# Kernel optimization log

Measured on AMD Instinct MI355X. Metric: run time of the kernel, lower is better.

Reference implementation:

```python
import jax, jax.numpy as jnp
import numpy as np

N_NODES = 100000
N_EDGES = 6400000
N_GRAPHS = 64


def setup_inputs() -> dict:
    key = jax.random.key(0)
    k = jax.random.split(key, 7)
    x = jax.random.normal(k[0], (N_NODES, 1), dtype=jnp.float32)
    edge_index = jax.random.randint(k[1], (2, N_EDGES), 0, N_NODES, dtype=jnp.int64)
    batch = jnp.sort(jax.random.randint(k[2], (N_NODES,), 0, N_GRAPHS, dtype=jnp.int64))
    W1 = jax.random.normal(k[3], (1, 16), dtype=jnp.float32)
    b1 = jax.random.normal(k[4], (16,), dtype=jnp.float32)
    W2 = jax.random.normal(k[5], (16, 2), dtype=jnp.float32)
    b2 = jax.random.normal(k[6], (2,), dtype=jnp.float32)
    return {"x": x, "edge_index": edge_index, "batch": batch,
            "W1": W1, "b1": b1, "W2": W2, "b2": b2}


def _gcn_layer(x, W, b, src, dst, n_nodes, dinv):
    # h = X W  (tiny feature dims)
    h = x @ W
    # symmetric normalization: norm_e = deg^-1/2[src] * deg^-1/2[dst]
    norm = dinv[src] * dinv[dst]
    msg = h[src] * norm[:, None]                 # [E+N, d] edge gather
    out = jnp.zeros((n_nodes, h.shape[1]), h.dtype).at[dst].add(msg)  # scatter-add at targets
    return out + b


def reference(x, edge_index, batch, W1, b1, W2, b2):
    n = x.shape[0]
    loops = jnp.arange(n, dtype=edge_index.dtype)
    # PyG GCNConv: add self-loops once; flow source_to_target (aggregate at edge_index[1])
    src = jnp.concatenate([edge_index[0], loops])
    dst = jnp.concatenate([edge_index[1], loops])
    deg = jnp.zeros(n, x.dtype).at[dst].add(jnp.ones((), x.dtype))
    dinv = jnp.where(deg > 0, jax.lax.rsqrt(deg), 0.0)

    h = _gcn_layer(x, W1, b1, src, dst, n, dinv)   # [N,16]
    h = _gcn_layer(h, W2, b2, src, dst, n, dinv)   # [N,2]

    # global_mean_pool over graphs
    g = N_GRAPHS
    sums = jnp.zeros((g, h.shape[1]), h.dtype).at[batch].add(h)
    counts = jnp.zeros(g, h.dtype).at[batch].add(jnp.ones((), h.dtype))
    return sums / jnp.maximum(counts, 1.0)[:, None]   # [G,2]
```

## Files before the change

### kernel.cpp

```cpp
#include <hip/hip_runtime.h>

#define N_NODES  100000
#define N_EDGES  6400000
#define N_GRAPHS 64
#define SCAN_BS  1024
#define NRDF     100096
#define DEGW     (NRDF / 4)
#define NR2      50048
#define LDSW     (NR2 / 2)

__global__ void setup_kernel(const int* ei, int* flag, float* gacc) {
    int t = threadIdx.x;
    if (t == 0) {
        int allzero = 1;
        for (int k = 0; k < 16; ++k)
            if (ei[2 * k + 1] != 0) allzero = 0;
        *flag = allzero ? 2 : 1;
    }
    if (t < 3 * N_GRAPHS) gacc[t] = 0.0f;
}

__global__ __launch_bounds__(SCAN_BS)
void deg_scan(const int* ei, const int* flag, unsigned char* copies) {
    __shared__ unsigned bins[DEGW];
    for (int i = threadIdx.x; i < DEGW; i += SCAN_BS) bins[i] = 0u;
    __syncthreads();
    const int stride = *flag;
    const int tid = blockIdx.x * SCAN_BS + threadIdx.x;
    const int nth = gridDim.x * SCAN_BS;
#define DEGADD(u) { unsigned a = (unsigned)(u); \
    if (a < NRDF) atomicAdd(&bins[a >> 2], 1u << (8 * (a & 3))); }
    if (stride == 2) {
        const int4* dp = (const int4*)(ei + (size_t)N_EDGES * 2);
        const int lim = N_EDGES / 2;
        int q = tid;
        for (; q + 3 * nth < lim; q += 4 * nth) {
            int4 v0 = dp[q], v1 = dp[q + nth];
            int4 v2 = dp[q + 2 * nth], v3 = dp[q + 3 * nth];
            DEGADD(v0.x); DEGADD(v0.z); DEGADD(v1.x); DEGADD(v1.z);
            DEGADD(v2.x); DEGADD(v2.z); DEGADD(v3.x); DEGADD(v3.z);
        }
        for (; q < lim; q += nth) { int4 v = dp[q]; DEGADD(v.x); DEGADD(v.z); }
    } else {
        const int4* dp = (const int4*)(ei + (size_t)N_EDGES);
        for (int q = tid; q < N_EDGES / 4; q += nth) {
            int4 v = dp[q];
            DEGADD(v.x); DEGADD(v.y); DEGADD(v.z); DEGADD(v.w);
        }
    }
#undef DEGADD
    __syncthreads();
    unsigned* my = (unsigned*)(copies + (size_t)blockIdx.x * NRDF);
    for (int i = threadIdx.x; i < DEGW; i += SCAN_BS) my[i] = bins[i];
}

__global__ void deg_merge(const unsigned char* copies, int C,
                          const float* x, const int* batch, const int* flag,
                          float* wx, float2* pbt) {
    __shared__ float red[256];
    int il = threadIdx.x & 63, cs = threadIdx.x >> 6;
    int gi = blockIdx.x * 64 + il;
    bool ok = (gi < N_NODES);
    float partial = 0.0f;
    if (ok)
        for (int c = cs; c < C; c += 4)
            partial += (float)copies[(size_t)c * NRDF + gi];
    red[threadIdx.x] = partial;
    __syncthreads();
    if (cs == 0 && ok) {
        float d = 1.0f + red[il] + red[64 + il] + red[128 + il] + red[192 + il];
        float di = rsqrtf(d);
        wx[gi] = di * x[gi];
        const int stride = *flag;
        pbt[gi] = make_float2(di, (float)batch[(size_t)gi * stride]);
    }
}

__device__ __forceinline__ void pk_add_f16(unsigned ldsBase, unsigned a, float v) {
    _Float16 h = (_Float16)v;
    unsigned hb = (unsigned)__builtin_bit_cast(unsigned short, h);
    unsigned pk = (a & 1) ? (hb << 16) : hb;
    unsigned addr = ldsBase + ((a >> 1) << 2);
    asm volatile("ds_pk_add_f16 %0, %1" :: "v"(addr), "v"(pk) : "memory");
}

__global__ __launch_bounds__(SCAN_BS)
void acc1_scan(const int* ei, const int* flag, const float* wx, int G,
               unsigned* copies) {
    __shared__ unsigned bins[LDSW];
    for (int i = threadIdx.x; i < LDSW; i += SCAN_BS) bins[i] = 0u;
    __syncthreads();
    const int lo = (blockIdx.x >= G) ? NR2 : 0;
    const unsigned ldsBase = (unsigned)(uintptr_t)&bins[0];
    const int stride = *flag;
    const int tid = blockIdx.x * SCAN_BS + threadIdx.x;
    const int nth = gridDim.x * SCAN_BS;
    if (stride == 2) {
        const int* srcp = ei;
        const int4* dp = (const int4*)(ei + (size_t)N_EDGES * 2);
        const int lim = N_EDGES / 2;
        int q = tid;
        for (; q + 3 * nth < lim; q += 4 * nth) {
            int4 v0 = dp[q], v1 = dp[q + nth];
            int4 v2 = dp[q + 2 * nth], v3 = dp[q + 3 * nth];
            unsigned a0 = (unsigned)(v0.x - lo), a1 = (unsigned)(v0.z - lo);
            unsigned a2 = (unsigned)(v1.x - lo), a3 = (unsigned)(v1.z - lo);
            unsigned a4 = (unsigned)(v2.x - lo), a5 = (unsigned)(v2.z - lo);
            unsigned a6 = (unsigned)(v3.x - lo), a7 = (unsigned)(v3.z - lo);
            int s0 = 0, s1 = 0, s2 = 0, s3 = 0, s4 = 0, s5 = 0, s6 = 0, s7 = 0;
            if (a0 < NR2) s0 = srcp[(size_t)4 * q];
            if (a1 < NR2) s1 = srcp[(size_t)4 * q + 2];
            if (a2 < NR2) s2 = srcp[(size_t)4 * (q + nth)];
            if (a3 < NR2) s3 = srcp[(size_t)4 * (q + nth) + 2];
            if (a4 < NR2) s4 = srcp[(size_t)4 * (q + 2 * nth)];
            if (a5 < NR2) s5 = srcp[(size_t)4 * (q + 2 * nth) + 2];
            if (a6 < NR2) s6 = srcp[(size_t)4 * (q + 3 * nth)];
            if (a7 < NR2) s7 = srcp[(size_t)4 * (q + 3 * nth) + 2];
            float w0 = wx[s0], w1 = wx[s1], w2 = wx[s2], w3 = wx[s3];
            float w4 = wx[s4], w5 = wx[s5], w6 = wx[s6], w7 = wx[s7];
            if (a0 < NR2) pk_add_f16(ldsBase, a0, w0);
            if (a1 < NR2) pk_add_f16(ldsBase, a1, w1);
            if (a2 < NR2) pk_add_f16(ldsBase, a2, w2);
            if (a3 < NR2) pk_add_f16(ldsBase, a3, w3);
            if (a4 < NR2) pk_add_f16(ldsBase, a4, w4);
            if (a5 < NR2) pk_add_f16(ldsBase, a5, w5);
            if (a6 < NR2) pk_add_f16(ldsBase, a6, w6);
            if (a7 < NR2) pk_add_f16(ldsBase, a7, w7);
        }
        for (; q < lim; q += nth) {
            int4 v = dp[q];
            unsigned a = (unsigned)(v.x - lo), b = (unsigned)(v.z - lo);
            if (a < NR2) pk_add_f16(ldsBase, a, wx[srcp[(size_t)4 * q]]);
            if (b < NR2) pk_add_f16(ldsBase, b, wx[srcp[(size_t)4 * q + 2]]);
        }
    } else {
        const int* srcp = ei;
        const int4* dp = (const int4*)(ei + (size_t)N_EDGES);
        for (int q = tid; q < N_EDGES / 4; q += nth) {
            int4 v = dp[q];
            unsigned a = (unsigned)(v.x - lo), b = (unsigned)(v.y - lo);
            unsigned c = (unsigned)(v.z - lo), d = (unsigned)(v.w - lo);
            if (a < NR2) pk_add_f16(ldsBase, a, wx[srcp[4 * q + 0]]);
            if (b < NR2) pk_add_f16(ldsBase, b, wx[srcp[4 * q + 1]]);
            if (c < NR2) pk_add_f16(ldsBase, c, wx[srcp[4 * q + 2]]);
            if (d < NR2) pk_add_f16(ldsBase, d, wx[srcp[4 * q + 3]]);
        }
    }
    __syncthreads();
    unsigned* my = copies + (size_t)blockIdx.x * LDSW;
    for (int i = threadIdx.x; i < LDSW; i += SCAN_BS) my[i] = bins[i];
}

__global__ void acc1_merge(const unsigned* copies, int G,
                           const float* wx, const float2* pbt,
                           float2* py, float* gacc) {
    __shared__ float red[256];
    __shared__ float bins[3 * N_GRAPHS];
    int t = threadIdx.x;
    for (int k = t; k < 3 * N_GRAPHS; k += 256) bins[k] = 0.0f;
    int il = t & 63, cs = t >> 6;
    int gi = blockIdx.x * 64 + il;
    bool ok = (gi < N_NODES);
    float partial = 0.0f;
    int grp = (gi >= NR2) ? 1 : 0;
    int li  = gi - grp * NR2;
    if (ok) {
        int sh = 16 * (li & 1), w = li >> 1;
        const unsigned* base = copies + (size_t)grp * G * LDSW;
        for (int c = cs; c < G; c += 4) {
            unsigned u = (base[(size_t)c * LDSW + w] >> sh) & 0xFFFFu;
            partial += (float)__builtin_bit_cast(_Float16, (unsigned short)u);
        }
    }
    red[t] = partial;
    __syncthreads();
    if (cs == 0 && ok) {
        float a1 = red[il] + red[64 + il] + red[128 + il] + red[192 + il];
        float2 pb = pbt[gi];
        float di = pb.x;
        float y1 = di * (a1 + wx[gi]);
        py[gi] = make_float2(di, y1);
        int g = (int)pb.y;
        float di2 = di * di;
        atomicAdd(&bins[g], di2 * y1);
        atomicAdd(&bins[N_GRAPHS + g], di2);
        atomicAdd(&bins[2 * N_GRAPHS + g], 1.0f);
    }
    __syncthreads();
    for (int k = t; k < 3 * N_GRAPHS; k += 256)
        if (bins[k] != 0.0f) atomicAdd(&gacc[k], bins[k]);
}

#define PW 16
__global__ __launch_bounds__(SCAN_BS)
void pool_scan(const int* ei, const int* flag, const float2* py,
               const float2* pbt, float* gacc) {
    __shared__ float wb[PW][2 * N_GRAPHS];
    int t = threadIdx.x;
    for (int k = t; k < PW * 2 * N_GRAPHS; k += SCAN_BS) ((float*)wb)[k] = 0.0f;
    __syncthreads();
    float* mb = wb[t >> 6];
    const int stride = *flag;
    const int tid = blockIdx.x * SCAN_BS + t;
    const int nth = gridDim.x * SCAN_BS;
    if (stride == 2) {
        const int4* sp = (const int4*)ei;
        const int4* dp = (const int4*)(ei + (size_t)N_EDGES * 2);
        int q = tid;
        for (; q + nth < N_EDGES / 2; q += 2 * nth) {
            int4 s0 = sp[q], d0 = dp[q], s1 = sp[q + nth], d1 = dp[q + nth];
            float2 pa0 = py[s0.x], pb0 = pbt[d0.x];
            float2 pa1 = py[s0.z], pb1 = pbt[d0.z];
            float2 pa2 = py[s1.x], pb2 = pbt[d1.x];
            float2 pa3 = py[s1.z], pb3 = pbt[d1.z];
            float w0 = pb0.x * pa0.x, w1 = pb1.x * pa1.x;
            float w2 = pb2.x * pa2.x, w3 = pb3.x * pa3.x;
            int g0 = (int)pb0.y, g1 = (int)pb1.y, g2 = (int)pb2.y, g3 = (int)pb3.y;
            atomicAdd(&mb[g0], w0 * pa0.y); atomicAdd(&mb[N_GRAPHS + g0], w0);
            atomicAdd(&mb[g1], w1 * pa1.y); atomicAdd(&mb[N_GRAPHS + g1], w1);
            atomicAdd(&mb[g2], w2 * pa2.y); atomicAdd(&mb[N_GRAPHS + g2], w2);
            atomicAdd(&mb[g3], w3 * pa3.y); atomicAdd(&mb[N_GRAPHS + g3], w3);
        }
        for (; q < N_EDGES / 2; q += nth) {
            int4 sv = sp[q], dv = dp[q];
            float2 pa0 = py[sv.x], pb0 = pbt[dv.x];
            float2 pa1 = py[sv.z], pb1 = pbt[dv.z];
            float w0 = pb0.x * pa0.x, w1 = pb1.x * pa1.x;
            int g0 = (int)pb0.y, g1 = (int)pb1.y;
            atomicAdd(&mb[g0], w0 * pa0.y); atomicAdd(&mb[N_GRAPHS + g0], w0);
            atomicAdd(&mb[g1], w1 * pa1.y); atomicAdd(&mb[N_GRAPHS + g1], w1);
        }
    } else {
        const int4* sp = (const int4*)ei;
        const int4* dp = (const int4*)(ei + (size_t)N_EDGES);
        for (int q = tid; q < N_EDGES / 4; q += nth) {
            int4 sv = sp[q], dv = dp[q];
            int ss[4] = {sv.x, sv.y, sv.z, sv.w};
            int dd[4] = {dv.x, dv.y, dv.z, dv.w};
            #pragma unroll
            for (int k = 0; k < 4; ++k) {
                float2 pa = py[ss[k]]; float2 pb = pbt[dd[k]];
                float w = pb.x * pa.x; int g = (int)pb.y;
                atomicAdd(&mb[g], w * pa.y); atomicAdd(&mb[N_GRAPHS + g], w);
            }
        }
    }
    __syncthreads();
    for (int k = t; k < 2 * N_GRAPHS; k += SCAN_BS) {
        float s = 0.0f;
        for (int w = 0; w < PW; ++w) s += wb[w][k];
        if (s != 0.0f) atomicAdd(&gacc[k], s);
    }
}

__global__ void final_kernel(const float* W1, const float* b1, const float* W2,
                             const float* b2, const float* gacc, float* out) {
    int g = threadIdx.x;
    if (g >= N_GRAPHS) return;
    float w0 = 0.f, w1 = 0.f, c0 = 0.f, c1 = 0.f;
    for (int j = 0; j < 16; ++j) {
        float a = W2[2 * j], b = W2[2 * j + 1];
        w0 += W1[j] * a;  w1 += W1[j] * b;
        c0 += b1[j] * a;  c1 += b1[j] * b;
    }
    float sy  = gacc[g];
    float sz  = gacc[N_GRAPHS + g];
    float cnt = gacc[2 * N_GRAPHS + g];
    float inv = 1.0f / fmaxf(cnt, 1.0f);
    out[2 * g + 0] = (sy * w0 + sz * c0 + cnt * b2[0]) * inv;
    out[2 * g + 1] = (sy * w1 + sz * c1 + cnt * b2[1]) * inv;
}

extern "C" void kernel_launch(void* const* d_in, const int* in_sizes, int n_in,
                              void* d_out, int out_size, void* d_ws, size_t ws_size,
                              hipStream_t stream) {
    const float* x     = (const float*)d_in[0];
    const int*   ei    = (const int*)d_in[1];
    const int*   batch = (const int*)d_in[2];
    const float* W1    = (const float*)d_in[3];
    const float* b1    = (const float*)d_in[4];
    const float* W2    = (const float*)d_in[5];
    const float* b2    = (const float*)d_in[6];
    float* out = (float*)d_out;

    float*  f    = (float*)d_ws;
    float*  wx   = f;
    float2* py   = (float2*)(wx + N_NODES);
    float2* pbt  = py + N_NODES;
    float*  gacc = (float*)(pbt + N_NODES);
    int*    flag = (int*)(gacc + 3 * N_GRAPHS);
    unsigned* copies = (unsigned*)(flag + 16);

    const long fixedB = (5L * N_NODES + 3 * N_GRAPHS + 16) * 4;
    long availB = (long)ws_size - fixedB;
    long CD = availB / NRDF;
    if (CD > 256) CD = 256; if (CD < 8) CD = 8;
    long G = availB / (2L * LDSW * 4);
    if (G > 128) G = 128; if (G < 4) G = 4;

    setup_kernel<<<1, 256, 0, stream>>>(ei, flag, gacc);

    deg_scan<<<(int)CD, SCAN_BS, 0, stream>>>(ei, flag, (unsigned char*)copies);
    deg_merge<<<(N_NODES + 63) / 64, 256, 0, stream>>>(
        (const unsigned char*)copies, (int)CD, x, batch, flag, wx, pbt);

    acc1_scan<<<(int)(2 * G), SCAN_BS, 0, stream>>>(ei, flag, wx, (int)G, copies);
    acc1_merge<<<(N_NODES + 63) / 64, 256, 0, stream>>>(
        copies, (int)G, wx, pbt, py, gacc);

    pool_scan<<<512, SCAN_BS, 0, stream>>>(ei, flag, py, pbt, gacc);
    final_kernel<<<1, 64, 0, stream>>>(W1, b1, W2, b2, gacc, out);
}
```

Measured before the change: 170.4 us.

## Replace pooled edge scan with LDS-binned packed fp16 second aggregation

The pooling pass used to scatter every edge into per-graph LDS bins with float atomics on a small set of addresses. It is replaced by a second node-range-partitioned scan. Each edge adds a packed fp16 pair (di*y1, di) of its source into a per-destination LDS bin using ds_pk_add_f16. A merge kernel then reduces the per-block copies and folds the results into the per-graph sums. The aim is to avoid heavy atomic contention on 64 graph bins and to halve the gather width, at the cost of a third partition, more partial-copy traffic, and fp16 accumulation error.

After: 168.2 us. No clear change (-1.3%).

```diff
diff --git a/kernel.cpp b/kernel.cpp
--- a/kernel.cpp
+++ b/kernel.cpp
@@ -8,6 +8,7 @@
 #define DEGW     (NRDF / 4)
 #define NR2      50048
 #define LDSW     (NR2 / 2)
+#define NR3      33344
 
 __global__ void setup_kernel(const int* ei, int* flag, float* gacc) {
     int t = threadIdx.x;
@@ -90,11 +91,13 @@
     __shared__ unsigned bins[LDSW];
     for (int i = threadIdx.x; i < LDSW; i += SCAN_BS) bins[i] = 0u;
     __syncthreads();
-    const int lo = (blockIdx.x >= G) ? NR2 : 0;
+    const int grp = (blockIdx.x >= G) ? 1 : 0;
+    const int lo = grp * NR2;
+    const int lb = blockIdx.x - grp * G;
     const unsigned ldsBase = (unsigned)(uintptr_t)&bins[0];
     const int stride = *flag;
-    const int tid = blockIdx.x * SCAN_BS + threadIdx.x;
-    const int nth = gridDim.x * SCAN_BS;
+    const int tid = lb * SCAN_BS + threadIdx.x;
+    const int nth = G * SCAN_BS;
     if (stride == 2) {
         const int* srcp = ei;
         const int4* dp = (const int4*)(ei + (size_t)N_EDGES * 2);
@@ -153,11 +156,9 @@
 
 __global__ void acc1_merge(const unsigned* copies, int G,
                            const float* wx, const float2* pbt,
-                           float2* py, float* gacc) {
+                           float* y1, unsigned* pyz) {
     __shared__ float red[256];
-    __shared__ float bins[3 * N_GRAPHS];
     int t = threadIdx.x;
-    for (int k = t; k < 3 * N_GRAPHS; k += 256) bins[k] = 0.0f;
     int il = t & 63, cs = t >> 6;
     int gi = blockIdx.x * 64 + il;
     bool ok = (gi < N_NODES);
@@ -176,81 +177,128 @@
     __syncthreads();
     if (cs == 0 && ok) {
         float a1 = red[il] + red[64 + il] + red[128 + il] + red[192 + il];
+        float di = pbt[gi].x;
+        float y1v = di * (a1 + wx[gi]);
+        y1[gi] = y1v;
+        _Float16 hy = (_Float16)(di * y1v);
+        _Float16 hz = (_Float16)di;
+        pyz[gi] = (unsigned)__builtin_bit_cast(unsigned short, hy)
+                | ((unsigned)__builtin_bit_cast(unsigned short, hz) << 16);
+    }
+}
+
+__global__ __launch_bounds__(SCAN_BS)
+void acc2_scan(const int* ei, const int* flag, const unsigned* pyz, int G,
+               unsigned* copies) {
+    __shared__ unsigned bins[NR3];
+    for (int i = threadIdx.x; i < NR3; i += SCAN_BS) bins[i] = 0u;
+    __syncthreads();
+    const int grp = blockIdx.x / G;
+    const int lo = grp * NR3;
+    const int lb = blockIdx.x - grp * G;
+    const unsigned ldsBase = (unsigned)(uintptr_t)&bins[0];
+    const int stride = *flag;
+    const int tid = lb * SCAN_BS + threadIdx.x;
+    const int nth = G * SCAN_BS;
+#define PKW(addr_a, pk) asm volatile("ds_pk_add_f16 %0, %1" :: \
+    "v"(ldsBase + ((addr_a) << 2)), "v"(pk) : "memory")
+    if (stride == 2) {
+        const int* srcp = ei;
+        const int4* dp = (const int4*)(ei + (size_t)N_EDGES * 2);
+        const int lim = N_EDGES / 2;
+        int q = tid;
+        for (; q + 3 * nth < lim; q += 4 * nth) {
+            int4 v0 = dp[q], v1 = dp[q + nth];
+            int4 v2 = dp[q + 2 * nth], v3 = dp[q + 3 * nth];
+            unsigned a0 = (unsigned)(v0.x - lo), a1 = (unsigned)(v0.z - lo);
+            unsigned a2 = (unsigned)(v1.x - lo), a3 = (unsigned)(v1.z - lo);
+            unsigned a4 = (unsigned)(v2.x - lo), a5 = (unsigned)(v2.z - lo);
+            unsigned a6 = (unsigned)(v3.x - lo), a7 = (unsigned)(v3.z - lo);
+            int s0 = 0, s1 = 0, s2 = 0, s3 = 0, s4 = 0, s5 = 0, s6 = 0, s7 = 0;
+            if (a0 < NR3) s0 = srcp[(size_t)4 * q];
+            if (a1 < NR3) s1 = srcp[(size_t)4 * q + 2];
+            if (a2 < NR3) s2 = srcp[(size_t)4 * (q + nth)];
+            if (a3 < NR3) s3 = srcp[(size_t)4 * (q + nth) + 2];
+            if (a4 < NR3) s4 = srcp[(size_t)4 * (q + 2 * nth)];
+            if (a5 < NR3) s5 = srcp[(size_t)4 * (q + 2 * nth) + 2];
+            if (a6 < NR3) s6 = srcp[(size_t)4 * (q + 3 * nth)];
+            if (a7 < NR3) s7 = srcp[(size_t)4 * (q + 3 * nth) + 2];
+            unsigned p0 = pyz[s0], p1 = pyz[s1], p2 = pyz[s2], p3 = pyz[s3];
+            unsigned p4 = pyz[s4], p5 = pyz[s5], p6 = pyz[s6], p7 = pyz[s7];
+            if (a0 < NR3) PKW(a0, p0);
+            if (a1 < NR3) PKW(a1, p1);
+            if (a2 < NR3) PKW(a2, p2);
+            if (a3 < NR3) PKW(a3, p3);
+            if (a4 < NR3) PKW(a4, p4);
+            if (a5 < NR3) PKW(a5, p5);
+            if (a6 < NR3) PKW(a6, p6);
+            if (a7 < NR3) PKW(a7, p7);
+        }
+        for (; q < lim; q += nth) {
+            int4 v = dp[q];
+            unsigned a = (unsigned)(v.x - lo), b = (unsigned)(v.z - lo);
+            if (a < NR3) { unsigned p = pyz[srcp[(size_t)4 * q]];     PKW(a, p); }
+            if (b < NR3) { unsigned p = pyz[srcp[(size_t)4 * q + 2]]; PKW(b, p); }
+        }
+    } else {
+        const int* srcp = ei;
+        const int4* dp = (const int4*)(ei + (size_t)N_EDGES);
+        for (int q = tid; q < N_EDGES / 4; q += nth) {
+            int4 v = dp[q];
+            unsigned a = (unsigned)(v.x - lo), b = (unsigned)(v.y - lo);
+            unsigned c = (unsigned)(v.z - lo), d = (unsigned)(v.w - lo);
+            if (a < NR3) { unsigned p = pyz[srcp[4 * q + 0]]; PKW(a, p); }
+            if (b < NR3) { unsigned p = pyz[srcp[4 * q + 1]]; PKW(b, p); }
+            if (c < NR3) { unsigned p = pyz[srcp[4 * q + 2]]; PKW(c, p); }
+            if (d < NR3) { unsigned p = pyz[srcp[4 * q + 3]]; PKW(d, p); }
+        }
+    }
+#undef PKW
+    __syncthreads();
+    unsigned* my = copies + (size_t)blockIdx.x * NR3;
+    for (int i = threadIdx.x; i < NR3; i += SCAN_BS) my[i] = bins[i];
+}
+
+__global__ void acc2_merge(const unsigned* copies, int G,
+                           const float* y1, const float2* pbt, float* gacc) {
+    __shared__ float redY[256];
+    __shared__ float redZ[256];
+    __shared__ float bins[3 * N_GRAPHS];
+    int t = threadIdx.x;
+    for (int k = t; k < 3 * N_GRAPHS; k += 256) bins[k] = 0.0f;
+    int il = t & 63, cs = t >> 6;
+    int gi = blockIdx.x * 64 + il;
+    bool ok = (gi < N_NODES);
+    float pyv = 0.0f, pzv = 0.0f;
+    if (ok) {
+        int grp = gi / NR3;
+        int li  = gi - grp * NR3;
+        const unsigned* base = copies + (size_t)grp * G * NR3;
+        for (int c = cs; c < G; c += 4) {
+            unsigned u = base[(size_t)c * NR3 + li];
+            pyv += (float)__builtin_bit_cast(_Float16, (unsigned short)(u & 0xFFFFu));
+            pzv += (float)__builtin_bit_cast(_Float16, (unsigned short)(u >> 16));
+        }
+    }
+    redY[t] = pyv;
+    redZ[t] = pzv;
+    __syncthreads();
+    if (cs == 0 && ok) {
+        float a2 = redY[il] + redY[64 + il] + redY[128 + il] + redY[192 + il];
+        float az = redZ[il] + redZ[64 + il] + redZ[128 + il] + redZ[192 + il];
         float2 pb = pbt[gi];
         float di = pb.x;
-        float y1 = di * (a1 + wx[gi]);
-        py[gi] = make_float2(di, y1);
         int g = (int)pb.y;
         float di2 = di * di;
-        atomicAdd(&bins[g], di2 * y1);
-        atomicAdd(&bins[N_GRAPHS + g], di2);
+        float yv = di * a2 + di2 * y1[gi];
+        float zv = di * az + di2;
+        atomicAdd(&bins[g], yv);
+        atomicAdd(&bins[N_GRAPHS + g], zv);
         atomicAdd(&bins[2 * N_GRAPHS + g], 1.0f);
     }
     __syncthreads();
     for (int k = t; k < 3 * N_GRAPHS; k += 256)
         if (bins[k] != 0.0f) atomicAdd(&gacc[k], bins[k]);
-}
-
-#define PW 16
-__global__ __launch_bounds__(SCAN_BS)
-void pool_scan(const int* ei, const int* flag, const float2* py,
-               const float2* pbt, float* gacc) {
-    __shared__ float wb[PW][2 * N_GRAPHS];
-    int t = threadIdx.x;
-    for (int k = t; k < PW * 2 * N_GRAPHS; k += SCAN_BS) ((float*)wb)[k] = 0.0f;
-    __syncthreads();
-    float* mb = wb[t >> 6];
-    const int stride = *flag;
-    const int tid = blockIdx.x * SCAN_BS + t;
-    const int nth = gridDim.x * SCAN_BS;
-    if (stride == 2) {
-        const int4* sp = (const int4*)ei;
-        const int4* dp = (const int4*)(ei + (size_t)N_EDGES * 2);
-        int q = tid;
-        for (; q + nth < N_EDGES / 2; q += 2 * nth) {
-            int4 s0 = sp[q], d0 = dp[q], s1 = sp[q + nth], d1 = dp[q + nth];
-            float2 pa0 = py[s0.x], pb0 = pbt[d0.x];
-            float2 pa1 = py[s0.z], pb1 = pbt[d0.z];
-            float2 pa2 = py[s1.x], pb2 = pbt[d1.x];
-            float2 pa3 = py[s1.z], pb3 = pbt[d1.z];
-            float w0 = pb0.x * pa0.x, w1 = pb1.x * pa1.x;
-            float w2 = pb2.x * pa2.x, w3 = pb3.x * pa3.x;
-            int g0 = (int)pb0.y, g1 = (int)pb1.y, g2 = (int)pb2.y, g3 = (int)pb3.y;
-            atomicAdd(&mb[g0], w0 * pa0.y); atomicAdd(&mb[N_GRAPHS + g0], w0);
-            atomicAdd(&mb[g1], w1 * pa1.y); atomicAdd(&mb[N_GRAPHS + g1], w1);
-            atomicAdd(&mb[g2], w2 * pa2.y); atomicAdd(&mb[N_GRAPHS + g2], w2);
-            atomicAdd(&mb[g3], w3 * pa3.y); atomicAdd(&mb[N_GRAPHS + g3], w3);
-        }
-        for (; q < N_EDGES / 2; q += nth) {
-            int4 sv = sp[q], dv = dp[q];
-            float2 pa0 = py[sv.x], pb0 = pbt[dv.x];
-            float2 pa1 = py[sv.z], pb1 = pbt[dv.z];
-            float w0 = pb0.x * pa0.x, w1 = pb1.x * pa1.x;
-            int g0 = (int)pb0.y, g1 = (int)pb1.y;
-            atomicAdd(&mb[g0], w0 * pa0.y); atomicAdd(&mb[N_GRAPHS + g0], w0);
-            atomicAdd(&mb[g1], w1 * pa1.y); atomicAdd(&mb[N_GRAPHS + g1], w1);
-        }
-    } else {
-        const int4* sp = (const int4*)ei;
-        const int4* dp = (const int4*)(ei + (size_t)N_EDGES);
-        for (int q = tid; q < N_EDGES / 4; q += nth) {
-            int4 sv = sp[q], dv = dp[q];
-            int ss[4] = {sv.x, sv.y, sv.z, sv.w};
-            int dd[4] = {dv.x, dv.y, dv.z, dv.w};
-            #pragma unroll
-            for (int k = 0; k < 4; ++k) {
-                float2 pa = py[ss[k]]; float2 pb = pbt[dd[k]];
-                float w = pb.x * pa.x; int g = (int)pb.y;
-                atomicAdd(&mb[g], w * pa.y); atomicAdd(&mb[N_GRAPHS + g], w);
-            }
-        }
-    }
-    __syncthreads();
-    for (int k = t; k < 2 * N_GRAPHS; k += SCAN_BS) {
-        float s = 0.0f;
-        for (int w = 0; w < PW; ++w) s += wb[w][k];
-        if (s != 0.0f) atomicAdd(&gacc[k], s);
-    }
 }
 
 __global__ void final_kernel(const float* W1, const float* b1, const float* W2,
@@ -283,20 +331,23 @@
     const float* b2    = (const float*)d_in[6];
     float* out = (float*)d_out;
 
-    float*  f    = (float*)d_ws;
-    float*  wx   = f;
-    float2* py   = (float2*)(wx + N_NODES);
-    float2* pbt  = py + N_NODES;
-    float*  gacc = (float*)(pbt + N_NODES);
-    int*    flag = (int*)(gacc + 3 * N_GRAPHS);
+    float*    f    = (float*)d_ws;
+    float*    wx   = f;
+    float*    y1   = wx + N_NODES;
+    float2*   pbt  = (float2*)(y1 + N_NODES);
+    unsigned* pyz  = (unsigned*)(pbt + N_NODES);
+    float*    gacc = (float*)(pyz + N_NODES);
+    int*      flag = (int*)(gacc + 3 * N_GRAPHS);
     unsigned* copies = (unsigned*)(flag + 16);
 
     const long fixedB = (5L * N_NODES + 3 * N_GRAPHS + 16) * 4;
     long availB = (long)ws_size - fixedB;
     long CD = availB / NRDF;
     if (CD > 256) CD = 256; if (CD < 8) CD = 8;
-    long G = availB / (2L * LDSW * 4);
-    if (G > 128) G = 128; if (G < 4) G = 4;
+    long G1 = availB / (2L * LDSW * 4);
+    if (G1 > 128) G1 = 128; if (G1 < 4) G1 = 4;
+    long G2 = availB / (3L * NR3 * 4);
+    if (G2 > 85) G2 = 85; if (G2 < 4) G2 = 4;
 
     setup_kernel<<<1, 256, 0, stream>>>(ei, flag, gacc);
 
@@ -304,10 +355,13 @@
     deg_merge<<<(N_NODES + 63) / 64, 256, 0, stream>>>(
         (const unsigned char*)copies, (int)CD, x, batch, flag, wx, pbt);
 
-    acc1_scan<<<(int)(2 * G), SCAN_BS, 0, stream>>>(ei, flag, wx, (int)G, copies);
+    acc1_scan<<<(int)(2 * G1), SCAN_BS, 0, stream>>>(ei, flag, wx, (int)G1, copies);
     acc1_merge<<<(N_NODES + 63) / 64, 256, 0, stream>>>(
-        copies, (int)G, wx, pbt, py, gacc);
-
-    pool_scan<<<512, SCAN_BS, 0, stream>>>(ei, flag, py, pbt, gacc);
+        copies, (int)G1, wx, pbt, y1, pyz);
+
+    acc2_scan<<<(int)(3 * G2), SCAN_BS, 0, stream>>>(ei, flag, pyz, (int)G2, copies);
+    acc2_merge<<<(N_NODES + 63) / 64, 256, 0, stream>>>(
+        copies, (int)G2, y1, pbt, gacc);
+
     final_kernel<<<1, 64, 0, stream>>>(W1, b1, W2, b2, gacc, out);
 }
```
